# Kernel optimization log

Hardware: AMD Instinct MI355X
Metric: run time of the kernel (lower is better)

The kernel has to match this reference:

```python
import jax, jax.numpy as jnp
import numpy as np

N, B, D = 2048, 4, 2048   # seq_len, batch, embed_dim (sequence-first layout)
E = 2                     # expand_ratio
H = D // E                # number of heads
EPS = 1e-5


def setup_inputs() -> dict:
    key = jax.random.key(0)
    ks = jax.random.split(key, 3)
    x = jax.random.normal(ks[0], (N, B, D), dtype=jnp.float32)
    W_in = jax.random.normal(ks[1], (3 * D, D), dtype=jnp.float32) / np.sqrt(D).astype(np.float32)
    b_in = jnp.zeros((3 * D,), jnp.float32)
    W_out = jax.random.normal(ks[2], (D, D), dtype=jnp.float32) / np.sqrt(D).astype(np.float32)
    b_out = jnp.zeros((D,), jnp.float32)
    gamma = jnp.ones((D,), jnp.float32)
    beta = jnp.zeros((D,), jnp.float32)
    return {"x": x, "W_in": W_in, "b_in": b_in, "gamma": gamma, "beta": beta,
            "W_out": W_out, "b_out": b_out}


def _linear_scan(lam, u):
    # h_t = lam_t * h_{t-1} + u_t along time axis 0 (HgruRealFunction)
    def combine(c1, c2):
        a1, b1 = c1
        a2, b2 = c2
        return a1 * a2, a2 * b1 + b2
    _, h = jax.lax.associative_scan(combine, (lam, u), axis=0)
    return h


def _layernorm(x, gamma, beta):
    mu = jnp.mean(x, axis=-1, keepdims=True)
    var = jnp.var(x, axis=-1, keepdims=True)
    return (x - mu) * jax.lax.rsqrt(var + EPS) * gamma + beta


def reference(x, W_in, b_in, gamma, beta, W_out, b_out):
    n, b, d = x.shape
    feat = x @ W_in.T + b_in                       # (n,b,3d)
    inp, og, fg = jnp.split(feat, 3, axis=-1)
    inp = jax.nn.silu(inp)                         # act_fun = silu
    og = jax.nn.sigmoid(og)                        # uv_act_fun = sigmoid
    lam = jax.nn.sigmoid(fg)                       # lower_bound = 0 => lambda = sigmoid(F)

    inp = inp.reshape(n, b, H, E)
    og = og.reshape(n, b, H, E)
    lam = lam.reshape(n, b, H, E)

    # input = einsum('...hd,...he->...hde', 1-lambda, input)
    u = ((1.0 - lam)[..., :, None] * inp[..., None, :]).reshape(n, b, H * E * E)
    lam_f = jnp.broadcast_to(lam[..., :, None], (n, b, H, E, E)).reshape(n, b, H * E * E)

    s_fwd = _linear_scan(lam_f, u)
    s_rev = jnp.flip(_linear_scan(jnp.flip(lam_f, 0), jnp.flip(u, 0)), 0)
    s = (s_fwd + s_rev).reshape(n, b, H, E, E)

    o = jnp.einsum('nbhde,nbhd->nbhe', s, og).reshape(n, b, d)
    o = _layernorm(o, gamma, beta)
    return o @ W_out.T + b_out
```

## Files before the change

### kernel.cpp

```cpp
#include <hip/hip_runtime.h>
#include <hip/hip_bf16.h>

#define NSEQ 2048
#define NB   4
#define DIM  2048
#define HN   1024
#define FC   6144
#define MROWS 8192
#define CHUNKS 64
#define CLEN 32
#define NCH  4096

typedef __bf16 bf16x8_t __attribute__((ext_vector_type(8)));
typedef float  f32x4_t  __attribute__((ext_vector_type(4)));

__device__ __forceinline__ float sigm(float x){ return 1.f/(1.f + __expf(-x)); }
__device__ __forceinline__ float bflo(unsigned p){ return __uint_as_float(p << 16); }
__device__ __forceinline__ float bfhi(unsigned p){ return __uint_as_float(p & 0xffff0000u); }
__device__ __forceinline__ unsigned short f2bf(float f){
  union { __hip_bfloat16 h; unsigned short u; } cv;
  cv.h = __float2bfloat16(f);
  return cv.u;
}

__global__ __launch_bounds__(256) void cvt_bf16_4(const float4* __restrict__ in,
                                                  ushort4* __restrict__ out, int n4){
  int i = blockIdx.x * blockDim.x + threadIdx.x;
  int st = gridDim.x * blockDim.x;
  for (; i < n4; i += st){
    float4 v = in[i];
    ushort4 r;
    r.x = f2bf(v.x); r.y = f2bf(v.y); r.z = f2bf(v.z); r.w = f2bf(v.w);
    out[i] = r;
  }
}

__device__ __forceinline__ void gl_lds16(const void* g, void* l){
  __builtin_amdgcn_global_load_lds((const __attribute__((address_space(1))) void*)g,
                                   (__attribute__((address_space(3))) void*)l, 16, 0, 0);
}

template <typename OutT>
__global__ __launch_bounds__(256, 2) void gemm256x128(const __hip_bfloat16* __restrict__ A,
                                                      const __hip_bfloat16* __restrict__ B,
                                                      const float* __restrict__ bias,
                                                      OutT* __restrict__ C,
                                                      int M, int N, int K, int nbx){
  __shared__ __align__(16) __hip_bfloat16 smem[3*12288];
  const int tid  = threadIdx.x;
  const int wave = tid >> 6, lane = tid & 63;

  const int cpx = gridDim.x >> 3;
  const int wg  = (blockIdx.x & 7) * cpx + (blockIdx.x >> 3);
  const int bx = wg % nbx, by = wg / nbx;
  const int m0 = by * 256, n0 = bx * 128;

  const int wr = wave >> 1, wc = wave & 1;
  const int r  = lane & 15, q = lane >> 4;
  const int NT = K >> 5;

  int aoff[8], boff[4];
  #pragma unroll
  for (int f = 0; f < 8; ++f){
    int R = wr*128 + f*16 + r;
    aoff[f] = (R>>1)*64 + (((((R&1)<<2) | q) ^ ((R>>1)&7)) << 3);
  }
  #pragma unroll
  for (int n = 0; n < 4; ++n){
    int R = wc*64 + n*16 + r;
    boff[n] = (R>>1)*64 + (((((R&1)<<2) | q) ^ ((R>>1)&7)) << 3);
  }

  auto stage = [&](int kt, int bo){
    #pragma unroll
    for (int i = 0; i < 4; ++i){
      int g = i*256 + tid;
      int line = g >> 3, glog = (g & 7) ^ (line & 7);
      int row = line*2 + (glog >> 2), kg = glog & 3;
      gl_lds16(A + (size_t)(m0 + row)*K + kt + kg*8, smem + bo + g*8);
    }
    #pragma unroll
    for (int i = 0; i < 2; ++i){
      int g = i*256 + tid;
      int line = g >> 3, glog = (g & 7) ^ (line & 7);
      int row = line*2 + (glog >> 2), kg = glog & 3;
      gl_lds16(B + (size_t)(n0 + row)*K + kt + kg*8, smem + bo + 8192 + g*8);
    }
  };

  f32x4_t acc[8][4] = {};

  stage(0, 0);
  stage(32, 12288);
  for (int t = 0; t < NT; ++t){
    if (t + 1 < NT) asm volatile("s_waitcnt vmcnt(6)" ::: "memory");
    else            asm volatile("s_waitcnt vmcnt(0)" ::: "memory");
    __builtin_amdgcn_s_barrier();
    __builtin_amdgcn_sched_barrier(0);
    if (t + 2 < NT) stage((t+2)*32, ((t+2)%3)*12288);
    const __hip_bfloat16* Ab = smem + (t%3)*12288;
    const __hip_bfloat16* Bb = Ab + 8192;
    bf16x8_t af[8], bfr[4];
    #pragma unroll
    for (int fn = 0; fn < 4; ++fn)
      bfr[fn] = *reinterpret_cast<const bf16x8_t*>(Bb + boff[fn]);
    #pragma unroll
    for (int fm = 0; fm < 8; ++fm)
      af[fm] = *reinterpret_cast<const bf16x8_t*>(Ab + aoff[fm]);
    __builtin_amdgcn_s_setprio(1);
    #pragma unroll
    for (int fm = 0; fm < 8; ++fm)
      #pragma unroll
      for (int fn = 0; fn < 4; ++fn)
        acc[fm][fn] = __builtin_amdgcn_mfma_f32_16x16x32_bf16(af[fm], bfr[fn], acc[fm][fn], 0, 0, 0);
    __builtin_amdgcn_s_setprio(0);
  }

  #pragma unroll
  for (int fn = 0; fn < 4; ++fn){
    int col = n0 + wc*64 + fn*16 + r;
    float bv = bias[col];
    #pragma unroll
    for (int fm = 0; fm < 8; ++fm){
      int row0 = m0 + wr*128 + fm*16 + q*4;
      #pragma unroll
      for (int j = 0; j < 4; ++j){
        float v = acc[fm][fn][j] + bv;
        if constexpr (__is_same(OutT, float))
          C[(size_t)(row0 + j)*N + col] = v;
        else
          C[(size_t)(row0 + j)*N + col] = __float2bfloat16(v);
      }
    }
  }
}

struct SV { float l0, l1, u00, u01, u10, u11; };
__device__ __forceinline__ SV stepp(unsigned pi, unsigned pf){
  SV s;
  s.l0 = sigm(bflo(pf)); s.l1 = sigm(bfhi(pf));
  float i0 = bflo(pi), i1 = bfhi(pi);
  i0 *= sigm(i0); i1 *= sigm(i1);
  float a0 = 1.f - s.l0, a1 = 1.f - s.l1;
  s.u00 = a0*i0; s.u01 = a0*i1; s.u10 = a1*i0; s.u11 = a1*i1;
  return s;
}

__global__ __launch_bounds__(256) void scan_agg(const unsigned* __restrict__ feat,
    float* __restrict__ aggP, float4* __restrict__ aggHF, float4* __restrict__ aggHR){
  int ch = blockIdx.x*256 + threadIdx.x;
  int c  = blockIdx.y;
  int b = ch >> 10, h = ch & 1023;
  int base = b*3072 + h;
  int n0 = c*CLEN;
  unsigned spi[CLEN], spf[CLEN];
  float P0 = 1.f, P1 = 1.f;
  float f00=0,f01=0,f10=0,f11=0;
  #pragma unroll
  for (int t = 0; t < CLEN; ++t){
    int rowu = (n0+t)*12288 + base;
    spi[t] = feat[rowu];
    spf[t] = feat[rowu + 2048];
    SV s = stepp(spi[t], spf[t]);
    f00 = s.l0*f00 + s.u00; f01 = s.l0*f01 + s.u01;
    f10 = s.l1*f10 + s.u10; f11 = s.l1*f11 + s.u11;
    P0 *= s.l0; P1 *= s.l1;
  }
  float r00=0,r01=0,r10=0,r11=0;
  #pragma unroll
  for (int t = CLEN-1; t >= 0; --t){
    SV s = stepp(spi[t], spf[t]);
    r00 = s.l0*r00 + s.u00; r01 = s.l0*r01 + s.u01;
    r10 = s.l1*r10 + s.u10; r11 = s.l1*r11 + s.u11;
  }
  aggP[c*8192 + ch*2]     = P0;
  aggP[c*8192 + ch*2 + 1] = P1;
  aggHF[c*4096 + ch] = make_float4(f00,f01,f10,f11);
  aggHR[c*4096 + ch] = make_float4(r00,r01,r10,r11);
}

__global__ __launch_bounds__(256) void scan_carry(const float* __restrict__ aggP,
    const float* __restrict__ aggHF, const float* __restrict__ aggHR,
    float* __restrict__ cF, float* __restrict__ cR){
  int t  = blockIdx.x*256 + threadIdx.x;
  int pd = t >> 1;
  float s = 0.f;
  for (int c = 0; c < CHUNKS; ++c){
    cF[c*16384 + t] = s;
    s = aggP[c*8192 + pd]*s + aggHF[c*16384 + t];
  }
  s = 0.f;
  for (int c = CHUNKS-1; c >= 0; --c){
    cR[c*16384 + t] = s;
    s = aggP[c*8192 + pd]*s + aggHR[c*16384 + t];
  }
}

__global__ __launch_bounds__(256, 1) void scan_fr(const unsigned* __restrict__ feat,
    const float4* __restrict__ cF, const float4* __restrict__ cR,
    float2* __restrict__ o){
  int ch = blockIdx.x*256 + threadIdx.x;
  int c  = blockIdx.y;
  int b = ch >> 10, h = ch & 1023;
  int base = b*3072 + h;
  unsigned spi[CLEN], spf[CLEN], spo[CLEN];
  float2 accv[CLEN];
  {
    float4 hv = cF[c*4096 + ch];
    float h00=hv.x, h01=hv.y, h10=hv.z, h11=hv.w;
    #pragma unroll
    for (int t = 0; t < CLEN; ++t){
      int rowu = (c*CLEN + t)*12288 + base;
      spi[t] = feat[rowu];
      spo[t] = feat[rowu + 1024];
      spf[t] = feat[rowu + 2048];
      SV s = stepp(spi[t], spf[t]);
      h00 = s.l0*h00 + s.u00; h01 = s.l0*h01 + s.u01;
      h10 = s.l1*h10 + s.u10; h11 = s.l1*h11 + s.u11;
      float g0 = sigm(bflo(spo[t])), g1 = sigm(bfhi(spo[t]));
      accv[t] = make_float2(g0*h00 + g1*h10, g0*h01 + g1*h11);
    }
  }
  {
    float4 hv = cR[c*4096 + ch];
    float h00=hv.x, h01=hv.y, h10=hv.z, h11=hv.w;
    #pragma unroll
    for (int t = CLEN-1; t >= 0; --t){
      SV s = stepp(spi[t], spf[t]);
      h00 = s.l0*h00 + s.u00; h01 = s.l0*h01 + s.u01;
      h10 = s.l1*h10 + s.u10; h11 = s.l1*h11 + s.u11;
      float g0 = sigm(bflo(spo[t])), g1 = sigm(bfhi(spo[t]));
      accv[t].x += g0*h00 + g1*h10;
      accv[t].y += g0*h01 + g1*h11;
    }
  }
  #pragma unroll
  for (int t = 0; t < CLEN; ++t)
    o[((c*CLEN + t)*NB + b)*1024 + h] = accv[t];
}

__global__ __launch_bounds__(256) void layernorm_k(const float* __restrict__ o,
    const float* __restrict__ gamma, const float* __restrict__ beta,
    __hip_bfloat16* __restrict__ out){
  int row = blockIdx.x, t = threadIdx.x;
  const float4* x = (const float4*)(o + (size_t)row*DIM);
  float4 a = x[t], b = x[t + 256];
  float s  = (a.x + a.y) + (a.z + a.w) + (b.x + b.y) + (b.z + b.w);
  float ss = (a.x*a.x + a.y*a.y) + (a.z*a.z + a.w*a.w)
           + (b.x*b.x + b.y*b.y) + (b.z*b.z + b.w*b.w);
  #pragma unroll
  for (int off = 32; off > 0; off >>= 1){
    s  += __shfl_down(s, off);
    ss += __shfl_down(ss, off);
  }
  __shared__ float red[8];
  int wv = t >> 6, ln = t & 63;
  if (ln == 0){ red[wv] = s; red[4 + wv] = ss; }
  __syncthreads();
  float S  = (red[0] + red[1]) + (red[2] + red[3]);
  float SS = (red[4] + red[5]) + (red[6] + red[7]);
  float mu = S * (1.f/DIM);
  float rs = rsqrtf(SS * (1.f/DIM) - mu*mu + 1e-5f);
  const float4* gp = (const float4*)gamma;
  const float4* bp = (const float4*)beta;
  float4 g0 = gp[t], g1 = gp[t + 256], be0 = bp[t], be1 = bp[t + 256];
  ushort4* op = (ushort4*)(out + (size_t)row*DIM);
  ushort4 r0, r1;
  r0.x = f2bf((a.x - mu)*rs*g0.x + be0.x);
  r0.y = f2bf((a.y - mu)*rs*g0.y + be0.y);
  r0.z = f2bf((a.z - mu)*rs*g0.z + be0.z);
  r0.w = f2bf((a.w - mu)*rs*g0.w + be0.w);
  r1.x = f2bf((b.x - mu)*rs*g1.x + be1.x);
  r1.y = f2bf((b.y - mu)*rs*g1.y + be1.y);
  r1.z = f2bf((b.z - mu)*rs*g1.z + be1.z);
  r1.w = f2bf((b.w - mu)*rs*g1.w + be1.w);
  op[t] = r0; op[t + 256] = r1;
}

extern "C" void kernel_launch(void* const* d_in, const int* in_sizes, int n_in,
                              void* d_out, int out_size, void* d_ws, size_t ws_size,
                              hipStream_t stream){
  (void)in_sizes; (void)n_in; (void)out_size;
  const float* x     = (const float*)d_in[0];
  const float* W_in  = (const float*)d_in[1];
  const float* b_in  = (const float*)d_in[2];
  const float* gamma = (const float*)d_in[3];
  const float* beta  = (const float*)d_in[4];
  const float* W_out = (const float*)d_in[5];
  const float* b_out = (const float*)d_in[6];
  float* out = (float*)d_out;

  char* p = (char*)d_ws;
  auto carve = [&](size_t bytes) -> char* {
    char* r = p; p += (bytes + 255) & ~(size_t)255; return r;
  };
  __hip_bfloat16* feat = (__hip_bfloat16*)carve((size_t)MROWS*FC*2);
  char* U              = carve((size_t)MROWS*DIM*4);
  __hip_bfloat16* Wob  = (__hip_bfloat16*)carve((size_t)DIM*DIM*2);
  float* aggP  = (float*)carve((size_t)CHUNKS*8192*4);
  float* aggHF = (float*)carve((size_t)CHUNKS*16384*4);
  float* aggHR = (float*)carve((size_t)CHUNKS*16384*4);
  float* cF    = (float*)carve((size_t)CHUNKS*16384*4);
  float* cR    = (float*)carve((size_t)CHUNKS*16384*4);
  if ((size_t)(p - (char*)d_ws) > ws_size) return;

  __hip_bfloat16* xb  = (__hip_bfloat16*)U;
  __hip_bfloat16* Wib = (__hip_bfloat16*)(U + (size_t)MROWS*DIM*2);
  float* o            = (float*)U;
  __hip_bfloat16* oln = (__hip_bfloat16*)feat;

  cvt_bf16_4<<<2048, 256, 0, stream>>>((const float4*)x,     (ushort4*)xb,  MROWS*DIM/4);
  cvt_bf16_4<<<2048, 256, 0, stream>>>((const float4*)W_in,  (ushort4*)Wib, FC*DIM/4);
  cvt_bf16_4<<<1024, 256, 0, stream>>>((const float4*)W_out, (ushort4*)Wob, DIM*DIM/4);

  gemm256x128<__hip_bfloat16><<<1536, 256, 0, stream>>>(xb, Wib, b_in, feat, MROWS, FC, 2048, FC/128);

  scan_agg  <<<dim3(NCH/256, CHUNKS), 256, 0, stream>>>((const unsigned*)feat, aggP, (float4*)aggHF, (float4*)aggHR);
  scan_carry<<<64, 256, 0, stream>>>(aggP, aggHF, aggHR, cF, cR);
  scan_fr   <<<dim3(NCH/256, CHUNKS), 256, 0, stream>>>((const unsigned*)feat, (const float4*)cF, (const float4*)cR, (float2*)o);

  layernorm_k<<<MROWS, 256, 0, stream>>>(o, gamma, beta, oln);

  gemm256x128<float><<<512, 256, 0, stream>>>(oln, Wob, b_out, out, MROWS, DIM, 2048, DIM/128);
}
```

Measured before the change: 459.5 us.

## Load GEMM B operand straight from global into double-buffered registers, bypassing LDS

The GEMM kernel no longer stages the B tile through shared memory. Each wave now loads its own B fragments directly from global memory into two register buffers, prefetching step t+1 while step t computes, and only A stays in the triple-buffered LDS ring. This shrinks the LDS footprint and removes the B LDS writes and reads. In exchange, each B fragment is fetched from global once per wave rather than once per block, the loads are less coalesced, more VGPRs are used, and the new wait counts also force the next A stage to finish one iteration earlier, which shortens the pipeline depth.

Result: slower. 568.8 us (+23.8%).

```diff
diff --git a/kernel.cpp b/kernel.cpp
--- a/kernel.cpp
+++ b/kernel.cpp
@@ -46,7 +46,7 @@
                                                       const float* __restrict__ bias,
                                                       OutT* __restrict__ C,
                                                       int M, int N, int K, int nbx){
-  __shared__ __align__(16) __hip_bfloat16 smem[3*12288];
+  __shared__ __align__(16) __hip_bfloat16 smem[3*8192];
   const int tid  = threadIdx.x;
   const int wave = tid >> 6, lane = tid & 63;
 
@@ -59,17 +59,16 @@
   const int r  = lane & 15, q = lane >> 4;
   const int NT = K >> 5;
 
-  int aoff[8], boff[4];
+  int aoff[8];
   #pragma unroll
   for (int f = 0; f < 8; ++f){
     int R = wr*128 + f*16 + r;
     aoff[f] = (R>>1)*64 + (((((R&1)<<2) | q) ^ ((R>>1)&7)) << 3);
   }
-  #pragma unroll
-  for (int n = 0; n < 4; ++n){
-    int R = wc*64 + n*16 + r;
-    boff[n] = (R>>1)*64 + (((((R&1)<<2) | q) ^ ((R>>1)&7)) << 3);
-  }
+  const __hip_bfloat16* Bbase[4];
+  #pragma unroll
+  for (int fn = 0; fn < 4; ++fn)
+    Bbase[fn] = B + (size_t)(n0 + wc*64 + fn*16 + r)*K + q*8;
 
   auto stage = [&](int kt, int bo){
     #pragma unroll
@@ -79,31 +78,31 @@
       int row = line*2 + (glog >> 2), kg = glog & 3;
       gl_lds16(A + (size_t)(m0 + row)*K + kt + kg*8, smem + bo + g*8);
     }
-    #pragma unroll
-    for (int i = 0; i < 2; ++i){
-      int g = i*256 + tid;
-      int line = g >> 3, glog = (g & 7) ^ (line & 7);
-      int row = line*2 + (glog >> 2), kg = glog & 3;
-      gl_lds16(B + (size_t)(n0 + row)*K + kt + kg*8, smem + bo + 8192 + g*8);
-    }
   };
+  auto loadB = [&](int kt, bf16x8_t* dst){
+    #pragma unroll
+    for (int fn = 0; fn < 4; ++fn)
+      dst[fn] = *reinterpret_cast<const bf16x8_t*>(Bbase[fn] + kt);
+  };
 
   f32x4_t acc[8][4] = {};
+  bf16x8_t B0[4], B1[4];
 
   stage(0, 0);
-  stage(32, 12288);
-  for (int t = 0; t < NT; ++t){
-    if (t + 1 < NT) asm volatile("s_waitcnt vmcnt(6)" ::: "memory");
-    else            asm volatile("s_waitcnt vmcnt(0)" ::: "memory");
+  stage(32, 8192);
+  loadB(0, B0);
+  asm volatile("s_waitcnt vmcnt(0)" ::: "memory");
+
+  auto kbody = [&](int t, bf16x8_t* Buse, bf16x8_t* Bload){
     __builtin_amdgcn_s_barrier();
     __builtin_amdgcn_sched_barrier(0);
-    if (t + 2 < NT) stage((t+2)*32, ((t+2)%3)*12288);
-    const __hip_bfloat16* Ab = smem + (t%3)*12288;
-    const __hip_bfloat16* Bb = Ab + 8192;
-    bf16x8_t af[8], bfr[4];
-    #pragma unroll
-    for (int fn = 0; fn < 4; ++fn)
-      bfr[fn] = *reinterpret_cast<const bf16x8_t*>(Bb + boff[fn]);
+    if (t + 2 < NT) stage((t+2)*32, ((t+2)%3)*8192);
+    if (t + 1 < NT) loadB((t+1)*32, Bload);
+    if (t + 2 < NT)      asm volatile("s_waitcnt vmcnt(8)" ::: "memory");
+    else if (t + 1 < NT) asm volatile("s_waitcnt vmcnt(4)" ::: "memory");
+    else                 asm volatile("s_waitcnt vmcnt(0)" ::: "memory");
+    const __hip_bfloat16* Ab = smem + (t%3)*8192;
+    bf16x8_t af[8];
     #pragma unroll
     for (int fm = 0; fm < 8; ++fm)
       af[fm] = *reinterpret_cast<const bf16x8_t*>(Ab + aoff[fm]);
@@ -112,8 +111,13 @@
     for (int fm = 0; fm < 8; ++fm)
       #pragma unroll
       for (int fn = 0; fn < 4; ++fn)
-        acc[fm][fn] = __builtin_amdgcn_mfma_f32_16x16x32_bf16(af[fm], bfr[fn], acc[fm][fn], 0, 0, 0);
+        acc[fm][fn] = __builtin_amdgcn_mfma_f32_16x16x32_bf16(af[fm], Buse[fn], acc[fm][fn], 0, 0, 0);
     __builtin_amdgcn_s_setprio(0);
+  };
+
+  for (int t = 0; t < NT; t += 2){
+    kbody(t,     B0, B1);
+    kbody(t + 1, B1, B0);
   }
 
   #pragma unroll
```

## Fold LayerNorm into output GEMM epilogue and switch GEMM to double buffering

Applied to the files above, without the earlier changes.

The scan now writes its output as bf16 instead of fp32. A small rowstats kernel computes per-row rstd and rstd*mu, and gamma and beta are folded into a pre-scaled W_out with per-column sums. The output GEMM epilogue then applies the normalization algebraically, which removes the fp32 write and re-read of the full activation and the separate LayerNorm pass. The GEMM also drops from a triple-buffered to a double-buffered LDS pipeline with occupancy hint 3, trading prefetch depth for more resident blocks. Because the mean is subtracted after the bf16 matmul, this adds some risk of cancellation error.

After: 1.100 ms. +139.5%, slower.

```diff
diff --git a/kernel.cpp b/kernel.cpp
--- a/kernel.cpp
+++ b/kernel.cpp
@@ -17,6 +17,7 @@
 __device__ __forceinline__ float sigm(float x){ return 1.f/(1.f + __expf(-x)); }
 __device__ __forceinline__ float bflo(unsigned p){ return __uint_as_float(p << 16); }
 __device__ __forceinline__ float bfhi(unsigned p){ return __uint_as_float(p & 0xffff0000u); }
+__device__ __forceinline__ float ubf(unsigned short u){ return __uint_as_float(((unsigned)u) << 16); }
 __device__ __forceinline__ unsigned short f2bf(float f){
   union { __hip_bfloat16 h; unsigned short u; } cv;
   cv.h = __float2bfloat16(f);
@@ -40,13 +41,16 @@
                                    (__attribute__((address_space(3))) void*)l, 16, 0, 0);
 }
 
-template <typename OutT>
-__global__ __launch_bounds__(256, 2) void gemm256x128(const __hip_bfloat16* __restrict__ A,
+template <typename OutT, bool LNE>
+__global__ __launch_bounds__(256, 3) void gemm256x128(const __hip_bfloat16* __restrict__ A,
                                                       const __hip_bfloat16* __restrict__ B,
                                                       const float* __restrict__ bias,
+                                                      const float* __restrict__ rs,
+                                                      const float* __restrict__ rsmu,
+                                                      const float* __restrict__ S1,
                                                       OutT* __restrict__ C,
                                                       int M, int N, int K, int nbx){
-  __shared__ __align__(16) __hip_bfloat16 smem[3*12288];
+  __shared__ __align__(16) __hip_bfloat16 smem[2*12288];
   const int tid  = threadIdx.x;
   const int wave = tid >> 6, lane = tid & 63;
 
@@ -91,14 +95,15 @@
   f32x4_t acc[8][4] = {};
 
   stage(0, 0);
-  stage(32, 12288);
   for (int t = 0; t < NT; ++t){
-    if (t + 1 < NT) asm volatile("s_waitcnt vmcnt(6)" ::: "memory");
-    else            asm volatile("s_waitcnt vmcnt(0)" ::: "memory");
     __builtin_amdgcn_s_barrier();
-    __builtin_amdgcn_sched_barrier(0);
-    if (t + 2 < NT) stage((t+2)*32, ((t+2)%3)*12288);
-    const __hip_bfloat16* Ab = smem + (t%3)*12288;
+    if (t + 1 < NT){
+      stage((t+1)*32, ((t+1)&1)*12288);
+      asm volatile("s_waitcnt vmcnt(6)" ::: "memory");
+    } else {
+      asm volatile("s_waitcnt vmcnt(0)" ::: "memory");
+    }
+    const __hip_bfloat16* Ab = smem + (t&1)*12288;
     const __hip_bfloat16* Bb = Ab + 8192;
     bf16x8_t af[8], bfr[4];
     #pragma unroll
@@ -116,20 +121,43 @@
     __builtin_amdgcn_s_setprio(0);
   }
 
-  #pragma unroll
-  for (int fn = 0; fn < 4; ++fn){
-    int col = n0 + wc*64 + fn*16 + r;
-    float bv = bias[col];
+  if constexpr (LNE){
+    float S1c[4], Tc[4];
+    #pragma unroll
+    for (int fn = 0; fn < 4; ++fn){
+      int col = n0 + wc*64 + fn*16 + r;
+      S1c[fn] = S1[col];
+      Tc[fn]  = bias[col];
+    }
     #pragma unroll
     for (int fm = 0; fm < 8; ++fm){
-      int row0 = m0 + wr*128 + fm*16 + q*4;
       #pragma unroll
       for (int j = 0; j < 4; ++j){
-        float v = acc[fm][fn][j] + bv;
-        if constexpr (__is_same(OutT, float))
-          C[(size_t)(row0 + j)*N + col] = v;
-        else
-          C[(size_t)(row0 + j)*N + col] = __float2bfloat16(v);
+        int row = m0 + wr*128 + fm*16 + q*4 + j;
+        float rv = rs[row], rm = rsmu[row];
+        #pragma unroll
+        for (int fn = 0; fn < 4; ++fn){
+          int col = n0 + wc*64 + fn*16 + r;
+          C[(size_t)row*N + col] = (OutT)(rv*acc[fm][fn][j] - rm*S1c[fn] + Tc[fn]);
+        }
+      }
+    }
+  } else {
+    #pragma unroll
+    for (int fn = 0; fn < 4; ++fn){
+      int col = n0 + wc*64 + fn*16 + r;
+      float bv = bias[col];
+      #pragma unroll
+      for (int fm = 0; fm < 8; ++fm){
+        int row0 = m0 + wr*128 + fm*16 + q*4;
+        #pragma unroll
+        for (int j = 0; j < 4; ++j){
+          float v = acc[fm][fn][j] + bv;
+          if constexpr (__is_same(OutT, float))
+            C[(size_t)(row0 + j)*N + col] = v;
+          else
+            C[(size_t)(row0 + j)*N + col] = __float2bfloat16(v);
+        }
       }
     }
   }
@@ -198,7 +226,7 @@
 
 __global__ __launch_bounds__(256, 1) void scan_fr(const unsigned* __restrict__ feat,
     const float4* __restrict__ cF, const float4* __restrict__ cR,
-    float2* __restrict__ o){
+    unsigned* __restrict__ obf){
   int ch = blockIdx.x*256 + threadIdx.x;
   int c  = blockIdx.y;
   int b = ch >> 10, h = ch & 1023;
@@ -235,19 +263,24 @@
     }
   }
   #pragma unroll
-  for (int t = 0; t < CLEN; ++t)
-    o[((c*CLEN + t)*NB + b)*1024 + h] = accv[t];
-}
-
-__global__ __launch_bounds__(256) void layernorm_k(const float* __restrict__ o,
-    const float* __restrict__ gamma, const float* __restrict__ beta,
-    __hip_bfloat16* __restrict__ out){
+  for (int t = 0; t < CLEN; ++t){
+    unsigned pk = (unsigned)f2bf(accv[t].x) | ((unsigned)f2bf(accv[t].y) << 16);
+    obf[((c*CLEN + t)*NB + b)*1024 + h] = pk;
+  }
+}
+
+__global__ __launch_bounds__(256) void rowstats(const unsigned* __restrict__ obf,
+    float* __restrict__ rs, float* __restrict__ rsmu){
   int row = blockIdx.x, t = threadIdx.x;
-  const float4* x = (const float4*)(o + (size_t)row*DIM);
-  float4 a = x[t], b = x[t + 256];
-  float s  = (a.x + a.y) + (a.z + a.w) + (b.x + b.y) + (b.z + b.w);
-  float ss = (a.x*a.x + a.y*a.y) + (a.z*a.z + a.w*a.w)
-           + (b.x*b.x + b.y*b.y) + (b.z*b.z + b.w*b.w);
+  const uint4* p = (const uint4*)(obf + (size_t)row*1024);
+  uint4 v = p[t];
+  float s = 0.f, ss = 0.f;
+  unsigned w[4] = {v.x, v.y, v.z, v.w};
+  #pragma unroll
+  for (int i = 0; i < 4; ++i){
+    float a = bflo(w[i]), bb = bfhi(w[i]);
+    s += a + bb; ss += a*a + bb*bb;
+  }
   #pragma unroll
   for (int off = 32; off > 0; off >>= 1){
     s  += __shfl_down(s, off);
@@ -257,24 +290,49 @@
   int wv = t >> 6, ln = t & 63;
   if (ln == 0){ red[wv] = s; red[4 + wv] = ss; }
   __syncthreads();
-  float S  = (red[0] + red[1]) + (red[2] + red[3]);
-  float SS = (red[4] + red[5]) + (red[6] + red[7]);
-  float mu = S * (1.f/DIM);
-  float rs = rsqrtf(SS * (1.f/DIM) - mu*mu + 1e-5f);
-  const float4* gp = (const float4*)gamma;
-  const float4* bp = (const float4*)beta;
-  float4 g0 = gp[t], g1 = gp[t + 256], be0 = bp[t], be1 = bp[t + 256];
-  ushort4* op = (ushort4*)(out + (size_t)row*DIM);
-  ushort4 r0, r1;
-  r0.x = f2bf((a.x - mu)*rs*g0.x + be0.x);
-  r0.y = f2bf((a.y - mu)*rs*g0.y + be0.y);
-  r0.z = f2bf((a.z - mu)*rs*g0.z + be0.z);
-  r0.w = f2bf((a.w - mu)*rs*g0.w + be0.w);
-  r1.x = f2bf((b.x - mu)*rs*g1.x + be1.x);
-  r1.y = f2bf((b.y - mu)*rs*g1.y + be1.y);
-  r1.z = f2bf((b.z - mu)*rs*g1.z + be1.z);
-  r1.w = f2bf((b.w - mu)*rs*g1.w + be1.w);
-  op[t] = r0; op[t + 256] = r1;
+  if (t == 0){
+    float S  = (red[0] + red[1]) + (red[2] + red[3]);
+    float SS = (red[4] + red[5]) + (red[6] + red[7]);
+    float mu = S * (1.f/DIM);
+    float rv = rsqrtf(SS * (1.f/DIM) - mu*mu + 1e-5f);
+    rs[row] = rv;
+    rsmu[row] = rv * mu;
+  }
+}
+
+__global__ __launch_bounds__(256) void wprep(const float* __restrict__ W,
+    const float* __restrict__ gamma, const float* __restrict__ beta,
+    const float* __restrict__ bout, __hip_bfloat16* __restrict__ Wg,
+    float* __restrict__ S1, float* __restrict__ T){
+  int n = blockIdx.x, t = threadIdx.x;
+  const float4* wr_ = (const float4*)(W + (size_t)n*DIM);
+  const float4* gp  = (const float4*)gamma;
+  const float4* bp  = (const float4*)beta;
+  ushort4* og = (ushort4*)(Wg + (size_t)n*DIM);
+  float s1 = 0.f, s2 = 0.f;
+  #pragma unroll
+  for (int i = 0; i < 2; ++i){
+    int idx = t + i*256;
+    float4 w = wr_[idx], g = gp[idx], b = bp[idx];
+    ushort4 rr;
+    rr.x = f2bf(w.x*g.x); rr.y = f2bf(w.y*g.y); rr.z = f2bf(w.z*g.z); rr.w = f2bf(w.w*g.w);
+    og[idx] = rr;
+    s1 += ubf(rr.x) + ubf(rr.y) + ubf(rr.z) + ubf(rr.w);
+    s2 += b.x*w.x + b.y*w.y + b.z*w.z + b.w*w.w;
+  }
+  #pragma unroll
+  for (int off = 32; off > 0; off >>= 1){
+    s1 += __shfl_down(s1, off);
+    s2 += __shfl_down(s2, off);
+  }
+  __shared__ float red[8];
+  int wv = t >> 6, ln = t & 63;
+  if (ln == 0){ red[wv] = s1; red[4 + wv] = s2; }
+  __syncthreads();
+  if (t == 0){
+    S1[n] = (red[0] + red[1]) + (red[2] + red[3]);
+    T[n]  = (red[4] + red[5]) + (red[6] + red[7]) + bout[n];
+  }
 }
 
 extern "C" void kernel_launch(void* const* d_in, const int* in_sizes, int n_in,
@@ -296,30 +354,35 @@
   };
   __hip_bfloat16* feat = (__hip_bfloat16*)carve((size_t)MROWS*FC*2);
   char* U              = carve((size_t)MROWS*DIM*4);
-  __hip_bfloat16* Wob  = (__hip_bfloat16*)carve((size_t)DIM*DIM*2);
+  __hip_bfloat16* Wg   = (__hip_bfloat16*)carve((size_t)DIM*DIM*2);
   float* aggP  = (float*)carve((size_t)CHUNKS*8192*4);
   float* aggHF = (float*)carve((size_t)CHUNKS*16384*4);
   float* aggHR = (float*)carve((size_t)CHUNKS*16384*4);
   float* cF    = (float*)carve((size_t)CHUNKS*16384*4);
   float* cR    = (float*)carve((size_t)CHUNKS*16384*4);
+  float* rs    = (float*)carve((size_t)MROWS*4);
+  float* rsmu  = (float*)carve((size_t)MROWS*4);
+  float* S1    = (float*)carve((size_t)DIM*4);
+  float* T     = (float*)carve((size_t)DIM*4);
   if ((size_t)(p - (char*)d_ws) > ws_size) return;
 
   __hip_bfloat16* xb  = (__hip_bfloat16*)U;
   __hip_bfloat16* Wib = (__hip_bfloat16*)(U + (size_t)MROWS*DIM*2);
-  float* o            = (float*)U;
-  __hip_bfloat16* oln = (__hip_bfloat16*)feat;
-
-  cvt_bf16_4<<<2048, 256, 0, stream>>>((const float4*)x,     (ushort4*)xb,  MROWS*DIM/4);
-  cvt_bf16_4<<<2048, 256, 0, stream>>>((const float4*)W_in,  (ushort4*)Wib, FC*DIM/4);
-  cvt_bf16_4<<<1024, 256, 0, stream>>>((const float4*)W_out, (ushort4*)Wob, DIM*DIM/4);
-
-  gemm256x128<__hip_bfloat16><<<1536, 256, 0, stream>>>(xb, Wib, b_in, feat, MROWS, FC, 2048, FC/128);
+  unsigned* obf       = (unsigned*)U;
+
+  cvt_bf16_4<<<2048, 256, 0, stream>>>((const float4*)x,    (ushort4*)xb,  MROWS*DIM/4);
+  cvt_bf16_4<<<2048, 256, 0, stream>>>((const float4*)W_in, (ushort4*)Wib, FC*DIM/4);
+  wprep<<<DIM, 256, 0, stream>>>(W_out, gamma, beta, b_out, Wg, S1, T);
+
+  gemm256x128<__hip_bfloat16,false><<<1536, 256, 0, stream>>>(
+      xb, Wib, b_in, nullptr, nullptr, nullptr, feat, MROWS, FC, 2048, FC/128);
 
   scan_agg  <<<dim3(NCH/256, CHUNKS), 256, 0, stream>>>((const unsigned*)feat, aggP, (float4*)aggHF, (float4*)aggHR);
   scan_carry<<<64, 256, 0, stream>>>(aggP, aggHF, aggHR, cF, cR);
-  scan_fr   <<<dim3(NCH/256, CHUNKS), 256, 0, stream>>>((const unsigned*)feat, (const float4*)cF, (const float4*)cR, (float2*)o);
-
-  layernorm_k<<<MROWS, 256, 0, stream>>>(o, gamma, beta, oln);
-
-  gemm256x128<float><<<512, 256, 0, stream>>>(oln, Wob, b_out, out, MROWS, DIM, 2048, DIM/128);
-}
+  scan_fr   <<<dim3(NCH/256, CHUNKS), 256, 0, stream>>>((const unsigned*)feat, (const float4*)cF, (const float4*)cR, obf);
+
+  rowstats<<<MROWS, 256, 0, stream>>>(obf, rs, rsmu);
+
+  gemm256x128<float,true><<<512, 256, 0, stream>>>(
+      (const __hip_bfloat16*)obf, Wg, T, rs, rsmu, S1, out, MROWS, DIM, 2048, DIM/128);
+}
```
